# Kernel optimization log

Hardware: AMD Instinct MI355X
Metric: run time of the kernel (lower is better)

Reference implementation:

```python
import jax, jax.numpy as jnp
import numpy as np

B, S, D, H, E, F = 4, 2048, 1024, 16, 8, 4096
CAP_FACTOR = 1.25
DH = D // H


def setup_inputs() -> dict:
    key = jax.random.key(0)
    ks = jax.random.split(key, 8)
    s = 0.02
    return {
        "src": jax.random.normal(ks[0], (B, S, D), jnp.float32),
        "src_pad_mask": jnp.zeros((B, S), jnp.bool_),  # True = padding
        "ln1_g": jnp.ones((D,), jnp.float32),
        "ln1_b": jnp.zeros((D,), jnp.float32),
        "in_proj_w": jax.random.normal(ks[1], (3 * D, D), jnp.float32) * s,
        "in_proj_b": jnp.zeros((3 * D,), jnp.float32),
        "out_proj_w": jax.random.normal(ks[2], (D, D), jnp.float32) * s,
        "out_proj_b": jnp.zeros((D,), jnp.float32),
        "ln2_g": jnp.ones((D,), jnp.float32),
        "ln2_b": jnp.zeros((D,), jnp.float32),
        "router_w": jax.random.normal(ks[3], (D, E), jnp.float32) * s,
        "router_b": jnp.zeros((E,), jnp.float32),
        "w1": jax.random.normal(ks[4], (E, D, F), jnp.float32) * s,
        "b1": jnp.zeros((E, F), jnp.float32),
        "w2": jax.random.normal(ks[5], (E, F, D), jnp.float32) * s,
        "b2": jnp.zeros((E, D), jnp.float32),
    }


def _layernorm(x, g, b, eps=1e-5):
    m = jnp.mean(x, axis=-1, keepdims=True)
    v = jnp.mean(jnp.square(x - m), axis=-1, keepdims=True)
    return (x - m) * jax.lax.rsqrt(v + eps) * g + b


def _mha(x, pad_mask, in_proj_w, in_proj_b, out_proj_w, out_proj_b):
    qkv = x @ in_proj_w.T + in_proj_b                      # [B,S,3D]
    q, k, v = jnp.split(qkv, 3, axis=-1)
    q = q.reshape(B, S, H, DH)
    k = k.reshape(B, S, H, DH)
    v = v.reshape(B, S, H, DH)
    scores = jnp.einsum('bqhd,bkhd->bhqk', q, k) / np.sqrt(DH).astype(np.float32)
    scores = jnp.where(pad_mask[:, None, None, :], jnp.float32(-1e9), scores)
    attn = jax.nn.softmax(scores, axis=-1)
    out = jnp.einsum('bhqk,bkhd->bqhd', attn, v).reshape(B, S, D)
    return out @ out_proj_w.T + out_proj_b


def _switch(x, token_mask, router_w, router_b, w1, b1, w2, b2):
    N = B * S
    cap = int(CAP_FACTOR * N / E)
    tokens = x.reshape(N, D)
    tm = token_mask.reshape(N).astype(jnp.float32)
    logits = tokens @ router_w + router_b                  # [N,E]
    probs = jax.nn.softmax(logits, axis=-1)
    eidx = jnp.argmax(probs, axis=-1)                      # [N] top-1 expert
    gate = jnp.take_along_axis(probs, eidx[:, None], axis=1)[:, 0]
    oh = jax.nn.one_hot(eidx, E, dtype=jnp.float32) * tm[:, None]
    # position of each token within its expert's queue (1-based; 0 if masked)
    pos = jnp.sum(jnp.cumsum(oh, axis=0) * oh, axis=-1)
    keep = (pos > 0) & (pos <= cap)
    slot = eidx * cap + (pos - 1).astype(jnp.int32)        # flat slot in [E*cap)
    slot_scatter = jnp.where(keep, slot, E * cap)          # out-of-range => dropped
    keepf = keep.astype(jnp.float32)
    dispatch = jnp.zeros((E * cap, D), jnp.float32).at[slot_scatter].set(
        tokens * keepf[:, None], mode='drop')
    d = dispatch.reshape(E, cap, D)
    h = jax.nn.relu(jnp.einsum('ecd,edf->ecf', d, w1) + b1[:, None, :])
    o = jnp.einsum('ecf,efd->ecd', h, w2) + b2[:, None, :]
    slot_gather = jnp.where(keep, slot, 0)
    out = o.reshape(E * cap, D)[slot_gather] * (gate * keepf)[:, None]
    # aux losses over valid tokens
    denom = jnp.maximum(jnp.sum(tm), 1.0)
    f = jnp.sum(oh, axis=0) / denom                        # dispatch fraction per expert
    P = jnp.sum(probs * tm[:, None], axis=0) / denom       # mean router prob per expert
    lb_loss = E * jnp.sum(f * P)
    z_loss = jnp.sum(jnp.square(jax.nn.logsumexp(logits, axis=-1)) * tm) / denom
    return out.reshape(B, S, D), lb_loss, z_loss


def reference(src, src_pad_mask, ln1_g, ln1_b, in_proj_w, in_proj_b,
              out_proj_w, out_proj_b, ln2_g, ln2_b, router_w, router_b,
              w1, b1, w2, b2):
    x = _layernorm(src, ln1_g, ln1_b)
    attn = _mha(x, src_pad_mask, in_proj_w, in_proj_b, out_proj_w, out_proj_b)
    src1 = src + attn                                      # dropout=0.0
    token_mask = ~src_pad_mask
    x2 = _layernorm(src1, ln2_g, ln2_b)
    ffn, lb_loss, z_loss = _switch(x2, token_mask, router_w, router_b, w1, b1, w2, b2)
    src2 = src1 + ffn
    return (src2, lb_loss, z_loss)
```

## Files before the change

kernel.cpp:

```cpp
#include <hip/hip_runtime.h>

constexpr int cB = 4, cS = 2048, cD = 1024, cH = 16, cE = 8, cF = 4096;
constexpr int cN = cB * cS;
constexpr int cDH = 64;
constexpr int cCAP = 1280;
constexpr int cECAP = cE * cCAP;

typedef __attribute__((ext_vector_type(8))) short bf16x8;
typedef __attribute__((ext_vector_type(4))) float f32x4;
typedef __attribute__((ext_vector_type(4))) unsigned short u16x4;

__device__ inline unsigned short bf16_rne(float x) {
  unsigned u = __float_as_uint(x);
  u += 0x7FFF + ((u >> 16) & 1);
  return (unsigned short)(u >> 16);
}
__device__ inline float bf16_f(unsigned short h) {
  return __uint_as_float(((unsigned)h) << 16);
}

__global__ __launch_bounds__(256) void ln_kernel(const float* __restrict__ x,
                                                 const float* __restrict__ g,
                                                 const float* __restrict__ bb,
                                                 float* __restrict__ y) {
  __shared__ float red[8];
  const int row = blockIdx.x;
  const int t = threadIdx.x;
  const float4 v = ((const float4*)(x + (size_t)row * cD))[t];
  float s = v.x + v.y + v.z + v.w;
#pragma unroll
  for (int m = 32; m >= 1; m >>= 1) s += __shfl_xor(s, m, 64);
  if ((t & 63) == 0) red[t >> 6] = s;
  __syncthreads();
  const float mean = (red[0] + red[1] + red[2] + red[3]) * (1.0f / cD);
  const float dx = v.x - mean, dy = v.y - mean, dz = v.z - mean, dw = v.w - mean;
  float ss = dx * dx + dy * dy + dz * dz + dw * dw;
#pragma unroll
  for (int m = 32; m >= 1; m >>= 1) ss += __shfl_xor(ss, m, 64);
  if ((t & 63) == 0) red[4 + (t >> 6)] = ss;
  __syncthreads();
  const float var = (red[4] + red[5] + red[6] + red[7]) * (1.0f / cD);
  const float inv = rsqrtf(var + 1e-5f);
  const float4 gg = ((const float4*)g)[t];
  const float4 b4 = ((const float4*)bb)[t];
  float4 o;
  o.x = dx * inv * gg.x + b4.x;
  o.y = dy * inv * gg.y + b4.y;
  o.z = dz * inv * gg.z + b4.z;
  o.w = dw * inv * gg.w + b4.w;
  ((float4*)(y + (size_t)row * cD))[t] = o;
}

__global__ __launch_bounds__(256) void ln_split_kernel(
    const float* __restrict__ x, const float* __restrict__ g,
    const float* __restrict__ bb, unsigned short* __restrict__ yh,
    unsigned short* __restrict__ yl) {
  __shared__ float red[8];
  const int row = blockIdx.x;
  const int t = threadIdx.x;
  const float4 v = ((const float4*)(x + (size_t)row * cD))[t];
  float s = v.x + v.y + v.z + v.w;
#pragma unroll
  for (int m = 32; m >= 1; m >>= 1) s += __shfl_xor(s, m, 64);
  if ((t & 63) == 0) red[t >> 6] = s;
  __syncthreads();
  const float mean = (red[0] + red[1] + red[2] + red[3]) * (1.0f / cD);
  const float dx = v.x - mean, dy = v.y - mean, dz = v.z - mean, dw = v.w - mean;
  float ss = dx * dx + dy * dy + dz * dz + dw * dw;
#pragma unroll
  for (int m = 32; m >= 1; m >>= 1) ss += __shfl_xor(ss, m, 64);
  if ((t & 63) == 0) red[4 + (t >> 6)] = ss;
  __syncthreads();
  const float var = (red[4] + red[5] + red[6] + red[7]) * (1.0f / cD);
  const float inv = rsqrtf(var + 1e-5f);
  const float4 gg = ((const float4*)g)[t];
  const float4 b4 = ((const float4*)bb)[t];
  const float oa[4] = {dx * inv * gg.x + b4.x, dy * inv * gg.y + b4.y,
                       dz * inv * gg.z + b4.z, dw * inv * gg.w + b4.w};
  u16x4 hh, ll;
#pragma unroll
  for (int i = 0; i < 4; i++) {
    const unsigned short h16 = bf16_rne(oa[i]);
    hh[i] = h16;
    ll[i] = bf16_rne(oa[i] - bf16_f(h16));
  }
  *(u16x4*)(yh + (size_t)row * cD + t * 4) = hh;
  *(u16x4*)(yl + (size_t)row * cD + t * 4) = ll;
}

__global__ __launch_bounds__(256) void wsplit_kernel(const float* __restrict__ in,
                                                     unsigned short* __restrict__ hi,
                                                     unsigned short* __restrict__ lo,
                                                     int n4) {
  const int i = blockIdx.x * 256 + threadIdx.x;
  if (i >= n4) return;
  const float4 v = ((const float4*)in)[i];
  const float a[4] = {v.x, v.y, v.z, v.w};
  u16x4 hh, ll;
#pragma unroll
  for (int j = 0; j < 4; j++) {
    const unsigned short h16 = bf16_rne(a[j]);
    hh[j] = h16;
    ll[j] = bf16_rne(a[j] - bf16_f(h16));
  }
  *(u16x4*)(hi + (size_t)i * 4) = hh;
  *(u16x4*)(lo + (size_t)i * 4) = ll;
}

__global__ __launch_bounds__(256) void transpose_bf16_kernel(
    const float* __restrict__ in, unsigned short* __restrict__ outp, int Rr,
    int Cc) {
  __shared__ float T[64][65];
  const int z = blockIdx.z;
  in += (size_t)z * Rr * Cc;
  outp += (size_t)z * Rr * Cc;
  const int c0 = blockIdx.x * 64, r0 = blockIdx.y * 64;
  const int tid = threadIdx.x;
#pragma unroll
  for (int u = 0; u < 4; u++) {
    const int a = tid + u * 256;
    const int r = a >> 4, c4 = (a & 15) << 2;
    const float4 v = *(const float4*)(in + (size_t)(r0 + r) * Cc + c0 + c4);
    T[r][c4 + 0] = v.x;
    T[r][c4 + 1] = v.y;
    T[r][c4 + 2] = v.z;
    T[r][c4 + 3] = v.w;
  }
  __syncthreads();
#pragma unroll
  for (int u = 0; u < 4; u++) {
    const int a = tid + u * 256;
    const int c = a >> 4, r4 = (a & 15) << 2;
    u16x4 o;
#pragma unroll
    for (int i = 0; i < 4; i++) o[i] = bf16_rne(T[r4 + i][c]);
    *(u16x4*)(outp + (size_t)(c0 + c) * Rr + r0 + r4) = o;
  }
}

template <bool SPLIT, bool RELU, bool RESID, bool OUTBF16>
__global__ __launch_bounds__(256) void gemm_bf16(
    const unsigned short* __restrict__ Ah, const unsigned short* __restrict__ Al,
    size_t sA,
    const unsigned short* __restrict__ Bh, const unsigned short* __restrict__ Bl,
    size_t sB,
    const float* __restrict__ bias, size_t sBias,
    const float* __restrict__ R,
    void* __restrict__ Cv, size_t sC,
    int K, int lda, int ldb, int ldc) {
  __shared__ unsigned short AsH[128 * 40];
  __shared__ unsigned short BsH[128 * 40];
  __shared__ unsigned short AsL[SPLIT ? 128 * 40 : 8];
  __shared__ unsigned short BsL[SPLIT ? 128 * 40 : 8];
  const int z = blockIdx.z;
  Ah += (size_t)z * sA;
  Bh += (size_t)z * sB;
  if constexpr (SPLIT) {
    Al += (size_t)z * sA;
    Bl += (size_t)z * sB;
  }
  bias += (size_t)z * sBias;
  const int n0 = blockIdx.x * 128, m0 = blockIdx.y * 128;
  const int tid = threadIdx.x;
  const int wid = tid >> 6, lane = tid & 63;
  const int ln = lane & 15, quad = lane >> 4;
  const int wm = (wid >> 1) * 64, wn = (wid & 1) * 64;

  f32x4 acc[4][4];
#pragma unroll
  for (int i = 0; i < 4; i++)
#pragma unroll
    for (int j = 0; j < 4; j++) acc[i][j] = (f32x4){0.f, 0.f, 0.f, 0.f};

  for (int k0 = 0; k0 < K; k0 += 32) {
    __syncthreads();
#pragma unroll
    for (int u = 0; u < 2; u++) {
      const int c = tid + u * 256;
      const int row = c >> 2, ko = (c & 3) << 3;
      const int ld = row * 40 + ko;
      *(uint4*)&AsH[ld] = *(const uint4*)(Ah + (size_t)(m0 + row) * lda + k0 + ko);
      *(uint4*)&BsH[ld] = *(const uint4*)(Bh + (size_t)(n0 + row) * ldb + k0 + ko);
      if constexpr (SPLIT) {
        *(uint4*)&AsL[ld] = *(const uint4*)(Al + (size_t)(m0 + row) * lda + k0 + ko);
        *(uint4*)&BsL[ld] = *(const uint4*)(Bl + (size_t)(n0 + row) * ldb + k0 + ko);
      }
    }
    __syncthreads();
    bf16x8 bh[4], bl[4];
#pragma unroll
    for (int nt = 0; nt < 4; nt++) {
      bh[nt] = *(const bf16x8*)&BsH[(wn + nt * 16 + ln) * 40 + quad * 8];
      if constexpr (SPLIT)
        bl[nt] = *(const bf16x8*)&BsL[(wn + nt * 16 + ln) * 40 + quad * 8];
    }
#pragma unroll
    for (int mt = 0; mt < 4; mt++) {
      const bf16x8 ah = *(const bf16x8*)&AsH[(wm + mt * 16 + ln) * 40 + quad * 8];
      bf16x8 al;
      if constexpr (SPLIT)
        al = *(const bf16x8*)&AsL[(wm + mt * 16 + ln) * 40 + quad * 8];
#pragma unroll
      for (int nt = 0; nt < 4; nt++) {
        acc[mt][nt] =
            __builtin_amdgcn_mfma_f32_16x16x32_bf16(ah, bh[nt], acc[mt][nt], 0, 0, 0);
        if constexpr (SPLIT) {
          acc[mt][nt] =
              __builtin_amdgcn_mfma_f32_16x16x32_bf16(al, bh[nt], acc[mt][nt], 0, 0, 0);
          acc[mt][nt] =
              __builtin_amdgcn_mfma_f32_16x16x32_bf16(ah, bl[nt], acc[mt][nt], 0, 0, 0);
        }
      }
    }
  }
  float* Cf = nullptr;
  unsigned short* Cb = nullptr;
  if constexpr (OUTBF16)
    Cb = (unsigned short*)Cv + (size_t)z * sC;
  else
    Cf = (float*)Cv + (size_t)z * sC;
#pragma unroll
  for (int mt = 0; mt < 4; mt++) {
#pragma unroll
    for (int nt = 0; nt < 4; nt++) {
      const int col = n0 + wn + nt * 16 + ln;
      const float bv = bias[col];
#pragma unroll
      for (int r = 0; r < 4; r++) {
        const int row = m0 + wm + mt * 16 + quad * 4 + r;
        float v = acc[mt][nt][r] + bv;
        if constexpr (RELU) v = fmaxf(v, 0.f);
        if constexpr (RESID) v += R[(size_t)row * ldc + col];
        if constexpr (OUTBF16)
          Cb[(size_t)row * ldc + col] = bf16_rne(v);
        else
          Cf[(size_t)row * ldc + col] = v;
      }
    }
  }
}

__global__ __launch_bounds__(256) void qkv_split_kernel(
    const float* __restrict__ qkv,
    unsigned short* __restrict__ Qh, unsigned short* __restrict__ Ql,
    unsigned short* __restrict__ Kh, unsigned short* __restrict__ Kl,
    unsigned short* __restrict__ Vth, unsigned short* __restrict__ Vtl) {
  __shared__ float Vs[64 * 66];
  const int s0 = blockIdx.x << 6;
  const int h = blockIdx.y, b = blockIdx.z;
  const int tid = threadIdx.x;
  const size_t qkbase = ((size_t)(b * cH + h) * cS + s0) * cDH;
  const size_t vtbase = (size_t)(b * cH + h) * cDH * cS + s0;
#pragma unroll
  for (int u = 0; u < 4; u++) {
    const int a = tid + u * 256;
    const int r = a >> 4, c4 = (a & 15) << 2;
    const float* rowp = qkv + (size_t)(b * cS + s0 + r) * (3 * cD) + h * cDH + c4;
    const float4 qv = *(const float4*)(rowp);
    const float4 kv = *(const float4*)(rowp + cD);
    const float4 vv = *(const float4*)(rowp + 2 * cD);
    u16x4 hq, lq, hk, lk;
    const float qa[4] = {qv.x, qv.y, qv.z, qv.w};
    const float ka[4] = {kv.x, kv.y, kv.z, kv.w};
    const float va[4] = {vv.x, vv.y, vv.z, vv.w};
#pragma unroll
    for (int i = 0; i < 4; i++) {
      const unsigned short h16 = bf16_rne(qa[i]);
      hq[i] = h16;
      lq[i] = bf16_rne(qa[i] - bf16_f(h16));
      const unsigned short h17 = bf16_rne(ka[i]);
      hk[i] = h17;
      lk[i] = bf16_rne(ka[i] - bf16_f(h17));
      Vs[(c4 + i) * 66 + r] = va[i];
    }
    *(u16x4*)(Qh + qkbase + (size_t)r * cDH + c4) = hq;
    *(u16x4*)(Ql + qkbase + (size_t)r * cDH + c4) = lq;
    *(u16x4*)(Kh + qkbase + (size_t)r * cDH + c4) = hk;
    *(u16x4*)(Kl + qkbase + (size_t)r * cDH + c4) = lk;
  }
  __syncthreads();
#pragma unroll
  for (int u = 0; u < 4; u++) {
    const int a = tid + u * 256;
    const int dh = a >> 4, k4 = (a & 15) << 2;
    u16x4 hv, lv;
#pragma unroll
    for (int i = 0; i < 4; i++) {
      const float x = Vs[dh * 66 + k4 + i];
      const unsigned short h16 = bf16_rne(x);
      hv[i] = h16;
      lv[i] = bf16_rne(x - bf16_f(h16));
    }
    *(u16x4*)(Vth + vtbase + (size_t)dh * cS + k4) = hv;
    *(u16x4*)(Vtl + vtbase + (size_t)dh * cS + k4) = lv;
  }
}

__global__ __launch_bounds__(256) void attn_mfma_kernel(
    const unsigned short* __restrict__ Qh, const unsigned short* __restrict__ Ql,
    const unsigned short* __restrict__ Kh, const unsigned short* __restrict__ Kl,
    const unsigned short* __restrict__ Vth, const unsigned short* __restrict__ Vtl,
    const unsigned char* __restrict__ pad, unsigned short* __restrict__ Oh,
    unsigned short* __restrict__ Ol) {
  __shared__ unsigned short KsH[64 * 72];
  __shared__ unsigned short KsL[64 * 72];
  __shared__ unsigned short VsH[64 * 72];
  __shared__ unsigned short VsL[64 * 72];
  __shared__ unsigned short PsH[4 * 16 * 72];
  __shared__ unsigned short PsL[4 * 16 * 72];
  __shared__ float Mk[64];

  const int q0 = blockIdx.x << 6;
  const int h = blockIdx.y, b = blockIdx.z;
  const int tid = threadIdx.x;
  const int wid = tid >> 6, lane = tid & 63;
  const int ln = lane & 15, quad = lane >> 4;
  constexpr float SC2 = 0.125f * 1.4426950408889634f;

  const size_t bh = (size_t)(b * cH + h);
  const unsigned short* gKh = Kh + bh * cS * cDH;
  const unsigned short* gKl = Kl + bh * cS * cDH;
  const unsigned short* gVh = Vth + bh * cDH * cS;
  const unsigned short* gVl = Vtl + bh * cDH * cS;

  const size_t qbase = (bh * cS + q0 + wid * 16 + ln) * cDH;
  bf16x8 qh[2], ql[2];
#pragma unroll
  for (int ks = 0; ks < 2; ks++) {
    qh[ks] = *(const bf16x8*)(Qh + qbase + ks * 32 + quad * 8);
    ql[ks] = *(const bf16x8*)(Ql + qbase + ks * 32 + quad * 8);
  }

  f32x4 Oc[4];
  float mprev[4], lrun[4];
#pragma unroll
  for (int dt = 0; dt < 4; dt++) Oc[dt] = (f32x4){0.f, 0.f, 0.f, 0.f};
#pragma unroll
  for (int r = 0; r < 4; r++) {
    mprev[r] = -1e30f;
    lrun[r] = 0.f;
  }

  for (int kt = 0; kt < cS / 64; kt++) {
    const int k0 = kt << 6;
    __syncthreads();
#pragma unroll
    for (int u = 0; u < 2; u++) {
      const int a = tid + (u << 8);
      const int row = a >> 3, c8 = (a & 7) << 3;
      const int ld = row * 72 + c8;
      *(uint4*)&KsH[ld] = *(const uint4*)(gKh + (size_t)(k0 + row) * cDH + c8);
      *(uint4*)&KsL[ld] = *(const uint4*)(gKl + (size_t)(k0 + row) * cDH + c8);
      *(uint4*)&VsH[ld] = *(const uint4*)(gVh + (size_t)row * cS + k0 + c8);
      *(uint4*)&VsL[ld] = *(const uint4*)(gVl + (size_t)row * cS + k0 + c8);
    }
    if (tid < 64) Mk[tid] = pad[b * cS + k0 + tid] ? -1e30f : 0.0f;
    __syncthreads();

    f32x4 sac[4];
#pragma unroll
    for (int st = 0; st < 4; st++) {
      f32x4 acc = (f32x4){0.f, 0.f, 0.f, 0.f};
      const unsigned short* krH = &KsH[(st * 16 + ln) * 72];
      const unsigned short* krL = &KsL[(st * 16 + ln) * 72];
#pragma unroll
      for (int ks = 0; ks < 2; ks++) {
        const bf16x8 kh = *(const bf16x8*)(krH + ks * 32 + quad * 8);
        const bf16x8 kl = *(const bf16x8*)(krL + ks * 32 + quad * 8);
        acc = __builtin_amdgcn_mfma_f32_16x16x32_bf16(qh[ks], kh, acc, 0, 0, 0);
        acc = __builtin_amdgcn_mfma_f32_16x16x32_bf16(ql[ks], kh, acc, 0, 0, 0);
        acc = __builtin_amdgcn_mfma_f32_16x16x32_bf16(qh[ks], kl, acc, 0, 0, 0);
      }
      sac[st] = acc;
    }
    float sf[4][4];
#pragma unroll
    for (int st = 0; st < 4; st++) {
      const float ma = Mk[st * 16 + ln];
#pragma unroll
      for (int r = 0; r < 4; r++) sf[st][r] = sac[st][r] * SC2 + ma;
    }
#pragma unroll
    for (int r = 0; r < 4; r++) {
      float vm = fmaxf(fmaxf(sf[0][r], sf[1][r]), fmaxf(sf[2][r], sf[3][r]));
      vm = fmaxf(vm, __shfl_xor(vm, 1, 64));
      vm = fmaxf(vm, __shfl_xor(vm, 2, 64));
      vm = fmaxf(vm, __shfl_xor(vm, 4, 64));
      vm = fmaxf(vm, __shfl_xor(vm, 8, 64));
      const float mnew = fmaxf(mprev[r], vm);
      const float alpha = exp2f(mprev[r] - mnew);
      float rs = 0.f;
      unsigned short ph[4], pl[4];
#pragma unroll
      for (int st = 0; st < 4; st++) {
        const float p = exp2f(sf[st][r] - mnew);
        rs += p;
        const unsigned short h16 = bf16_rne(p);
        ph[st] = h16;
        pl[st] = bf16_rne(p - bf16_f(h16));
      }
      rs += __shfl_xor(rs, 1, 64);
      rs += __shfl_xor(rs, 2, 64);
      rs += __shfl_xor(rs, 4, 64);
      rs += __shfl_xor(rs, 8, 64);
      lrun[r] = lrun[r] * alpha + rs;
      mprev[r] = mnew;
#pragma unroll
      for (int dt = 0; dt < 4; dt++) Oc[dt][r] *= alpha;
      const int prow = wid * 1152 + (quad * 4 + r) * 72 + ln;
#pragma unroll
      for (int st = 0; st < 4; st++) {
        PsH[prow + st * 16] = ph[st];
        PsL[prow + st * 16] = pl[st];
      }
    }
    const unsigned short* pwH = PsH + wid * 1152 + ln * 72;
    const unsigned short* pwL = PsL + wid * 1152 + ln * 72;
#pragma unroll
    for (int dt = 0; dt < 4; dt++) {
      f32x4 acc = Oc[dt];
      const unsigned short* vrH = &VsH[(dt * 16 + ln) * 72];
      const unsigned short* vrL = &VsL[(dt * 16 + ln) * 72];
#pragma unroll
      for (int ks = 0; ks < 2; ks++) {
        const bf16x8 phv = *(const bf16x8*)(pwH + ks * 32 + quad * 8);
        const bf16x8 plv = *(const bf16x8*)(pwL + ks * 32 + quad * 8);
        const bf16x8 vh = *(const bf16x8*)(vrH + ks * 32 + quad * 8);
        const bf16x8 vl = *(const bf16x8*)(vrL + ks * 32 + quad * 8);
        acc = __builtin_amdgcn_mfma_f32_16x16x32_bf16(phv, vh, acc, 0, 0, 0);
        acc = __builtin_amdgcn_mfma_f32_16x16x32_bf16(plv, vh, acc, 0, 0, 0);
        acc = __builtin_amdgcn_mfma_f32_16x16x32_bf16(phv, vl, acc, 0, 0, 0);
      }
      Oc[dt] = acc;
    }
  }
  float inv[4];
#pragma unroll
  for (int r = 0; r < 4; r++) inv[r] = 1.0f / lrun[r];
#pragma unroll
  for (int dt = 0; dt < 4; dt++) {
#pragma unroll
    for (int r = 0; r < 4; r++) {
      const int tok = b * cS + q0 + wid * 16 + quad * 4 + r;
      const float v = Oc[dt][r] * inv[r];
      const unsigned short h16 = bf16_rne(v);
      const size_t idx = (size_t)tok * cD + h * cDH + dt * 16 + ln;
      Oh[idx] = h16;
      Ol[idx] = bf16_rne(v - bf16_f(h16));
    }
  }
}

__global__ __launch_bounds__(256) void router_kernel(
    const float* __restrict__ x2, const float* __restrict__ rw,
    const float* __restrict__ rb, const unsigned char* __restrict__ pad,
    float* __restrict__ gate, int* __restrict__ eidx, float* __restrict__ Psum,
    float* __restrict__ zsum) {
  __shared__ float Pacc[8];
  __shared__ float Zacc;
  if (threadIdx.x < 8) Pacc[threadIdx.x] = 0.f;
  if (threadIdx.x == 8) Zacc = 0.f;
  __syncthreads();
  const int tid = threadIdx.x, wid = tid >> 6, lane = tid & 63;
  const int e = lane & 7, dbase = lane >> 3;
  for (int tok = blockIdx.x * 4 + wid; tok < cN; tok += gridDim.x * 4) {
    const float* xr = x2 + (size_t)tok * cD;
    float partial = 0.f;
#pragma unroll 8
    for (int i = 0; i < cD / 8; i++) {
      const int d = dbase + i * 8;
      partial += xr[d] * rw[d * 8 + e];
    }
    partial += __shfl_xor(partial, 8, 64);
    partial += __shfl_xor(partial, 16, 64);
    partial += __shfl_xor(partial, 32, 64);
    const float logit = partial + rb[e];
    float mx = logit;
    mx = fmaxf(mx, __shfl_xor(mx, 1, 64));
    mx = fmaxf(mx, __shfl_xor(mx, 2, 64));
    mx = fmaxf(mx, __shfl_xor(mx, 4, 64));
    const float ex = __expf(logit - mx);
    float sm = ex;
    sm += __shfl_xor(sm, 1, 64);
    sm += __shfl_xor(sm, 2, 64);
    sm += __shfl_xor(sm, 4, 64);
    const float prob = ex / sm;
    float bv = logit;
    int bi = e;
#pragma unroll
    for (int m = 1; m < 8; m <<= 1) {
      const float ov = __shfl_xor(bv, m, 64);
      const int oi = __shfl_xor(bi, m, 64);
      if (ov > bv || (ov == bv && oi < bi)) {
        bv = ov;
        bi = oi;
      }
    }
    const float g = __shfl(prob, (lane & 0x38) | bi, 64);
    const bool valid = (pad[tok] == 0);
    if (lane == 0) {
      eidx[tok] = bi;
      gate[tok] = g;
    }
    if (valid) {
      if (lane < 8) atomicAdd(&Pacc[lane], prob);
      if (lane == 0) {
        const float lse = mx + logf(sm);
        atomicAdd(&Zacc, lse * lse);
      }
    }
  }
  __syncthreads();
  if (threadIdx.x < 8) atomicAdd(&Psum[threadIdx.x], Pacc[threadIdx.x]);
  if (threadIdx.x == 8) atomicAdd(zsum, Zacc);
}

__global__ __launch_bounds__(256) void scan_kernel(const int* __restrict__ eidx,
                                                   const unsigned char* __restrict__ pad,
                                                   int* __restrict__ slot,
                                                   int* __restrict__ counts) {
  __shared__ int cnt[256][8];
  const int t = threadIdx.x;
  int lc[8] = {0, 0, 0, 0, 0, 0, 0, 0};
  const int base = t * 32;
  for (int i = 0; i < 32; i++) {
    const int tok = base + i;
    if (!pad[tok]) lc[eidx[tok]]++;
  }
#pragma unroll
  for (int e2 = 0; e2 < 8; e2++) cnt[t][e2] = lc[e2];
  __syncthreads();
  if (t < 8) {
    int run = 0;
    for (int i = 0; i < 256; i++) {
      const int v = cnt[i][t];
      cnt[i][t] = run;
      run += v;
    }
    counts[t] = run;
  }
  __syncthreads();
  int off[8];
#pragma unroll
  for (int e2 = 0; e2 < 8; e2++) off[e2] = cnt[t][e2];
  for (int i = 0; i < 32; i++) {
    const int tok = base + i;
    if (!pad[tok]) {
      const int e2 = eidx[tok];
      const int p = off[e2]++;
      slot[tok] = (p < cCAP) ? (e2 * cCAP + p) : -1;
    } else {
      slot[tok] = -1;
    }
  }
}

__global__ __launch_bounds__(256) void dispatch_bf16_kernel(
    const float* __restrict__ x2, const int* __restrict__ slot,
    unsigned short* __restrict__ disp) {
  const int tok = blockIdx.x;
  const int s = slot[tok];
  if (s < 0) return;
  const float4 v = ((const float4*)(x2 + (size_t)tok * cD))[threadIdx.x];
  u16x4 o;
  o[0] = bf16_rne(v.x);
  o[1] = bf16_rne(v.y);
  o[2] = bf16_rne(v.z);
  o[3] = bf16_rne(v.w);
  *(u16x4*)(disp + (size_t)s * cD + threadIdx.x * 4) = o;
}

__global__ __launch_bounds__(256) void gather_kernel(const float* __restrict__ src1,
                                                     const float* __restrict__ o,
                                                     const int* __restrict__ slot,
                                                     const float* __restrict__ gate,
                                                     float* __restrict__ out) {
  const int tok = blockIdx.x;
  float4 r = ((const float4*)(src1 + (size_t)tok * cD))[threadIdx.x];
  const int s = slot[tok];
  if (s >= 0) {
    const float g = gate[tok];
    const float4 ov = ((const float4*)(o + (size_t)s * cD))[threadIdx.x];
    r.x += g * ov.x;
    r.y += g * ov.y;
    r.z += g * ov.z;
    r.w += g * ov.w;
  }
  ((float4*)(out + (size_t)tok * cD))[threadIdx.x] = r;
}

__global__ void loss_kernel(const int* __restrict__ counts,
                            const float* __restrict__ Psum,
                            const float* __restrict__ zsum,
                            float* __restrict__ out) {
  if (threadIdx.x == 0) {
    int tot = 0;
    for (int e2 = 0; e2 < 8; e2++) tot += counts[e2];
    const float denom = fmaxf((float)tot, 1.0f);
    float lp = 0.f;
    for (int e2 = 0; e2 < 8; e2++)
      lp += ((float)counts[e2] / denom) * (Psum[e2] / denom);
    out[0] = 8.0f * lp;
    out[1] = zsum[0] / denom;
  }
}

constexpr size_t OFF_A = 0;
constexpr size_t OFF_B = 25165824;
constexpr size_t OFF_XHL = 50331648;
constexpr size_t OFF_SRC1 = 58720256;
constexpr size_t OFF_X2O = 67108864;
constexpr size_t OFF_IPW = 77594624;
constexpr size_t OFF_OPW = 80740352;
constexpr size_t OFF_MISC = 81788928;

extern "C" void kernel_launch(void* const* d_in, const int* in_sizes, int n_in,
                              void* d_out, int out_size, void* d_ws, size_t ws_size,
                              hipStream_t stream) {
  (void)in_sizes; (void)n_in; (void)out_size; (void)ws_size;
  const float* src = (const float*)d_in[0];
  const unsigned char* pad = (const unsigned char*)d_in[1];
  const float* ln1_g = (const float*)d_in[2];
  const float* ln1_b = (const float*)d_in[3];
  const float* in_proj_w = (const float*)d_in[4];
  const float* in_proj_b = (const float*)d_in[5];
  const float* out_proj_w = (const float*)d_in[6];
  const float* out_proj_b = (const float*)d_in[7];
  const float* ln2_g = (const float*)d_in[8];
  const float* ln2_b = (const float*)d_in[9];
  const float* router_w = (const float*)d_in[10];
  const float* router_b = (const float*)d_in[11];
  const float* w1 = (const float*)d_in[12];
  const float* b1 = (const float*)d_in[13];
  const float* w2 = (const float*)d_in[14];
  const float* b2 = (const float*)d_in[15];
  float* out = (float*)d_out;
  float* w = (float*)d_ws;

  float* qkv = w + OFF_A;
  unsigned short* w1t = (unsigned short*)(w + OFF_A);
  unsigned short* w2t = (unsigned short*)(w + OFF_A);
  unsigned short* usB = (unsigned short*)(w + OFF_B);
  constexpr size_t SPN = (size_t)cN * cD;
  unsigned short* Qh = usB + 0 * SPN;
  unsigned short* Ql = usB + 1 * SPN;
  unsigned short* Kh = usB + 2 * SPN;
  unsigned short* Kl = usB + 3 * SPN;
  unsigned short* Vth = usB + 4 * SPN;
  unsigned short* Vtl = usB + 5 * SPN;
  unsigned short* hbuf16 = usB;
  unsigned short* xh = (unsigned short*)(w + OFF_XHL);
  unsigned short* xl = xh + SPN;
  unsigned short* Oh = xh;
  unsigned short* Ol = xh + SPN;
  unsigned short* disp16 = xh;
  float* src1 = w + OFF_SRC1;
  float* x2 = w + OFF_X2O;
  float* obuf = w + OFF_X2O;
  unsigned short* ipwh = (unsigned short*)(w + OFF_IPW);
  unsigned short* ipwl = ipwh + (size_t)3 * cD * cD;
  unsigned short* opwh = (unsigned short*)(w + OFF_OPW);
  unsigned short* opwl = opwh + (size_t)cD * cD;
  float* gate = w + OFF_MISC;
  int* eidx = (int*)(w + OFF_MISC + 8192);
  int* slot = (int*)(w + OFF_MISC + 16384);
  float* Psum = w + OFF_MISC + 24576;
  float* zsum = Psum + 8;
  int* counts = (int*)(Psum + 16);

  hipMemsetAsync(Psum, 0, 9 * sizeof(float), stream);

  ln_split_kernel<<<cN, 256, 0, stream>>>(src, ln1_g, ln1_b, xh, xl);
  wsplit_kernel<<<3072, 256, 0, stream>>>(in_proj_w, ipwh, ipwl, 786432);
  wsplit_kernel<<<1024, 256, 0, stream>>>(out_proj_w, opwh, opwl, 262144);
  gemm_bf16<true, false, false, false><<<dim3(24, 64, 1), 256, 0, stream>>>(
      xh, xl, 0, ipwh, ipwl, 0, in_proj_b, 0, nullptr, qkv, 0,
      cD, cD, cD, 3 * cD);
  qkv_split_kernel<<<dim3(cS / 64, cH, cB), 256, 0, stream>>>(
      qkv, Qh, Ql, Kh, Kl, Vth, Vtl);
  transpose_bf16_kernel<<<dim3(64, 16, 8), 256, 0, stream>>>(w1, w1t, cD, cF);
  attn_mfma_kernel<<<dim3(cS / 64, cH, cB), 256, 0, stream>>>(
      Qh, Ql, Kh, Kl, Vth, Vtl, pad, Oh, Ol);
  gemm_bf16<true, false, true, false><<<dim3(8, 64, 1), 256, 0, stream>>>(
      Oh, Ol, 0, opwh, opwl, 0, out_proj_b, 0, src, src1, 0,
      cD, cD, cD, cD);
  ln_kernel<<<cN, 256, 0, stream>>>(src1, ln2_g, ln2_b, x2);
  router_kernel<<<256, 256, 0, stream>>>(x2, router_w, router_b, pad, gate, eidx,
                                         Psum, zsum);
  scan_kernel<<<1, 256, 0, stream>>>(eidx, pad, slot, counts);
  dispatch_bf16_kernel<<<cN, 256, 0, stream>>>(x2, slot, disp16);
  gemm_bf16<false, true, false, true><<<dim3(32, 10, 8), 256, 0, stream>>>(
      disp16, nullptr, (size_t)cCAP * cD, w1t, nullptr, (size_t)cD * cF,
      b1, cF, nullptr, hbuf16, (size_t)cCAP * cF, cD, cD, cD, cF);
  transpose_bf16_kernel<<<dim3(16, 64, 8), 256, 0, stream>>>(w2, w2t, cF, cD);
  gemm_bf16<false, false, false, false><<<dim3(8, 10, 8), 256, 0, stream>>>(
      hbuf16, nullptr, (size_t)cCAP * cF, w2t, nullptr, (size_t)cF * cD,
      b2, cD, nullptr, obuf, (size_t)cCAP * cD, cF, cF, cF, cD);
  gather_kernel<<<cN, 256, 0, stream>>>(src1, obuf, slot, gate, out);
  loss_kernel<<<1, 64, 0, stream>>>(counts, Psum, zsum, out + (size_t)cN * cD);
}
```

Measured before the change: 1.488 ms.

## Fuse QKV split into GEMM epilogue and transpose attention MFMA operands

Measured after the change: 1.419 ms. 4.6% less time.

```diff
diff --git a/kernel.cpp b/kernel.cpp
--- a/kernel.cpp
+++ b/kernel.cpp
@@ -4,7 +4,6 @@
 constexpr int cN = cB * cS;
 constexpr int cDH = 64;
 constexpr int cCAP = 1280;
-constexpr int cECAP = cE * cCAP;
 
 typedef __attribute__((ext_vector_type(8))) short bf16x8;
 typedef __attribute__((ext_vector_type(4))) float f32x4;
@@ -138,7 +137,7 @@
   }
 }
 
-template <bool SPLIT, bool RELU, bool RESID, bool OUTBF16>
+template <bool SPLIT, bool RELU, bool RESID, int OUT>
 __global__ __launch_bounds__(256) void gemm_bf16(
     const unsigned short* __restrict__ Ah, const unsigned short* __restrict__ Al,
     size_t sA,
@@ -147,7 +146,10 @@
     const float* __restrict__ bias, size_t sBias,
     const float* __restrict__ R,
     void* __restrict__ Cv, size_t sC,
-    int K, int lda, int ldb, int ldc) {
+    int K, int lda, int ldb, int ldc,
+    unsigned short* __restrict__ Qh, unsigned short* __restrict__ Ql,
+    unsigned short* __restrict__ Kh, unsigned short* __restrict__ Kl,
+    unsigned short* __restrict__ Vth, unsigned short* __restrict__ Vtl) {
   __shared__ unsigned short AsH[128 * 40];
   __shared__ unsigned short BsH[128 * 40];
   __shared__ unsigned short AsL[SPLIT ? 128 * 40 : 8];
@@ -213,86 +215,73 @@
       }
     }
   }
-  float* Cf = nullptr;
-  unsigned short* Cb = nullptr;
-  if constexpr (OUTBF16)
-    Cb = (unsigned short*)Cv + (size_t)z * sC;
-  else
-    Cf = (float*)Cv + (size_t)z * sC;
-#pragma unroll
-  for (int mt = 0; mt < 4; mt++) {
-#pragma unroll
-    for (int nt = 0; nt < 4; nt++) {
-      const int col = n0 + wn + nt * 16 + ln;
-      const float bv = bias[col];
-#pragma unroll
-      for (int r = 0; r < 4; r++) {
-        const int row = m0 + wm + mt * 16 + quad * 4 + r;
-        float v = acc[mt][nt][r] + bv;
-        if constexpr (RELU) v = fmaxf(v, 0.f);
-        if constexpr (RESID) v += R[(size_t)row * ldc + col];
-        if constexpr (OUTBF16)
-          Cb[(size_t)row * ldc + col] = bf16_rne(v);
-        else
-          Cf[(size_t)row * ldc + col] = v;
-      }
-    }
-  }
-}
-
-__global__ __launch_bounds__(256) void qkv_split_kernel(
-    const float* __restrict__ qkv,
-    unsigned short* __restrict__ Qh, unsigned short* __restrict__ Ql,
-    unsigned short* __restrict__ Kh, unsigned short* __restrict__ Kl,
-    unsigned short* __restrict__ Vth, unsigned short* __restrict__ Vtl) {
-  __shared__ float Vs[64 * 66];
-  const int s0 = blockIdx.x << 6;
-  const int h = blockIdx.y, b = blockIdx.z;
-  const int tid = threadIdx.x;
-  const size_t qkbase = ((size_t)(b * cH + h) * cS + s0) * cDH;
-  const size_t vtbase = (size_t)(b * cH + h) * cDH * cS + s0;
-#pragma unroll
-  for (int u = 0; u < 4; u++) {
-    const int a = tid + u * 256;
-    const int r = a >> 4, c4 = (a & 15) << 2;
-    const float* rowp = qkv + (size_t)(b * cS + s0 + r) * (3 * cD) + h * cDH + c4;
-    const float4 qv = *(const float4*)(rowp);
-    const float4 kv = *(const float4*)(rowp + cD);
-    const float4 vv = *(const float4*)(rowp + 2 * cD);
-    u16x4 hq, lq, hk, lk;
-    const float qa[4] = {qv.x, qv.y, qv.z, qv.w};
-    const float ka[4] = {kv.x, kv.y, kv.z, kv.w};
-    const float va[4] = {vv.x, vv.y, vv.z, vv.w};
-#pragma unroll
-    for (int i = 0; i < 4; i++) {
-      const unsigned short h16 = bf16_rne(qa[i]);
-      hq[i] = h16;
-      lq[i] = bf16_rne(qa[i] - bf16_f(h16));
-      const unsigned short h17 = bf16_rne(ka[i]);
-      hk[i] = h17;
-      lk[i] = bf16_rne(ka[i] - bf16_f(h17));
-      Vs[(c4 + i) * 66 + r] = va[i];
-    }
-    *(u16x4*)(Qh + qkbase + (size_t)r * cDH + c4) = hq;
-    *(u16x4*)(Ql + qkbase + (size_t)r * cDH + c4) = lq;
-    *(u16x4*)(Kh + qkbase + (size_t)r * cDH + c4) = hk;
-    *(u16x4*)(Kl + qkbase + (size_t)r * cDH + c4) = lk;
-  }
-  __syncthreads();
-#pragma unroll
-  for (int u = 0; u < 4; u++) {
-    const int a = tid + u * 256;
-    const int dh = a >> 4, k4 = (a & 15) << 2;
-    u16x4 hv, lv;
-#pragma unroll
-    for (int i = 0; i < 4; i++) {
-      const float x = Vs[dh * 66 + k4 + i];
-      const unsigned short h16 = bf16_rne(x);
-      hv[i] = h16;
-      lv[i] = bf16_rne(x - bf16_f(h16));
-    }
-    *(u16x4*)(Vth + vtbase + (size_t)dh * cS + k4) = hv;
-    *(u16x4*)(Vtl + vtbase + (size_t)dh * cS + k4) = lv;
+  if constexpr (OUT == 2) {
+#pragma unroll
+    for (int mt = 0; mt < 4; mt++) {
+      const int row0 = m0 + wm + mt * 16 + quad * 4;
+      const int b_ = row0 >> 11, s0_ = row0 & 2047;
+      const size_t bbase = (size_t)b_ * cH * cS * cDH;
+#pragma unroll
+      for (int nt = 0; nt < 4; nt++) {
+        const int col = n0 + wn + nt * 16 + ln;
+        const float bv = bias[col];
+        const int sec = col >> 10;
+        const int f = col & 1023;
+        const int hh = f >> 6, d = f & 63;
+        const size_t bh_off = bbase + (size_t)hh * cS * cDH;
+        float vals[4];
+#pragma unroll
+        for (int r = 0; r < 4; r++) vals[r] = acc[mt][nt][r] + bv;
+        if (sec == 2) {
+          u16x4 hi4, lo4;
+#pragma unroll
+          for (int r = 0; r < 4; r++) {
+            const unsigned short h16 = bf16_rne(vals[r]);
+            hi4[r] = h16;
+            lo4[r] = bf16_rne(vals[r] - bf16_f(h16));
+          }
+          const size_t idx = bh_off + (size_t)d * cS + s0_;
+          *(u16x4*)(Vth + idx) = hi4;
+          *(u16x4*)(Vtl + idx) = lo4;
+        } else {
+          unsigned short* dsth = (sec == 0) ? Qh : Kh;
+          unsigned short* dstl = (sec == 0) ? Ql : Kl;
+#pragma unroll
+          for (int r = 0; r < 4; r++) {
+            const unsigned short h16 = bf16_rne(vals[r]);
+            const size_t idx = bh_off + (size_t)(s0_ + r) * cDH + d;
+            dsth[idx] = h16;
+            dstl[idx] = bf16_rne(vals[r] - bf16_f(h16));
+          }
+        }
+      }
+    }
+  } else {
+    float* Cf = nullptr;
+    unsigned short* Cb = nullptr;
+    if constexpr (OUT == 1)
+      Cb = (unsigned short*)Cv + (size_t)z * sC;
+    else
+      Cf = (float*)Cv + (size_t)z * sC;
+#pragma unroll
+    for (int mt = 0; mt < 4; mt++) {
+#pragma unroll
+      for (int nt = 0; nt < 4; nt++) {
+        const int col = n0 + wn + nt * 16 + ln;
+        const float bv = bias[col];
+#pragma unroll
+        for (int r = 0; r < 4; r++) {
+          const int row = m0 + wm + mt * 16 + quad * 4 + r;
+          float v = acc[mt][nt][r] + bv;
+          if constexpr (RELU) v = fmaxf(v, 0.f);
+          if constexpr (RESID) v += R[(size_t)row * ldc + col];
+          if constexpr (OUT == 1)
+            Cb[(size_t)row * ldc + col] = bf16_rne(v);
+          else
+            Cf[(size_t)row * ldc + col] = v;
+        }
+      }
+    }
   }
 }
 
@@ -332,14 +321,9 @@
   }
 
   f32x4 Oc[4];
-  float mprev[4], lrun[4];
 #pragma unroll
   for (int dt = 0; dt < 4; dt++) Oc[dt] = (f32x4){0.f, 0.f, 0.f, 0.f};
-#pragma unroll
-  for (int r = 0; r < 4; r++) {
-    mprev[r] = -1e30f;
-    lrun[r] = 0.f;
-  }
+  float mprev = -1e30f, lrun = 0.f;
 
   for (int kt = 0; kt < cS / 64; kt++) {
     const int k0 = kt << 6;
@@ -357,7 +341,7 @@
     if (tid < 64) Mk[tid] = pad[b * cS + k0 + tid] ? -1e30f : 0.0f;
     __syncthreads();
 
-    f32x4 sac[4];
+    float sf[4][4];
 #pragma unroll
     for (int st = 0; st < 4; st++) {
       f32x4 acc = (f32x4){0.f, 0.f, 0.f, 0.f};
@@ -367,52 +351,54 @@
       for (int ks = 0; ks < 2; ks++) {
         const bf16x8 kh = *(const bf16x8*)(krH + ks * 32 + quad * 8);
         const bf16x8 kl = *(const bf16x8*)(krL + ks * 32 + quad * 8);
-        acc = __builtin_amdgcn_mfma_f32_16x16x32_bf16(qh[ks], kh, acc, 0, 0, 0);
-        acc = __builtin_amdgcn_mfma_f32_16x16x32_bf16(ql[ks], kh, acc, 0, 0, 0);
-        acc = __builtin_amdgcn_mfma_f32_16x16x32_bf16(qh[ks], kl, acc, 0, 0, 0);
-      }
-      sac[st] = acc;
-    }
-    float sf[4][4];
+        acc = __builtin_amdgcn_mfma_f32_16x16x32_bf16(kh, qh[ks], acc, 0, 0, 0);
+        acc = __builtin_amdgcn_mfma_f32_16x16x32_bf16(kl, qh[ks], acc, 0, 0, 0);
+        acc = __builtin_amdgcn_mfma_f32_16x16x32_bf16(kh, ql[ks], acc, 0, 0, 0);
+      }
+      const float4 mkv = *(const float4*)&Mk[st * 16 + quad * 4];
+      sf[st][0] = acc[0] * SC2 + mkv.x;
+      sf[st][1] = acc[1] * SC2 + mkv.y;
+      sf[st][2] = acc[2] * SC2 + mkv.z;
+      sf[st][3] = acc[3] * SC2 + mkv.w;
+    }
+    float vm = -1e30f;
+#pragma unroll
+    for (int st = 0; st < 4; st++)
+#pragma unroll
+      for (int r = 0; r < 4; r++) vm = fmaxf(vm, sf[st][r]);
+    vm = fmaxf(vm, __shfl_xor(vm, 16, 64));
+    vm = fmaxf(vm, __shfl_xor(vm, 32, 64));
+    const float mnew = fmaxf(mprev, vm);
+    const float alpha = exp2f(mprev - mnew);
+    float rs = 0.f;
+    u16x4 phv[4], plv[4];
 #pragma unroll
     for (int st = 0; st < 4; st++) {
-      const float ma = Mk[st * 16 + ln];
-#pragma unroll
-      for (int r = 0; r < 4; r++) sf[st][r] = sac[st][r] * SC2 + ma;
-    }
-#pragma unroll
-    for (int r = 0; r < 4; r++) {
-      float vm = fmaxf(fmaxf(sf[0][r], sf[1][r]), fmaxf(sf[2][r], sf[3][r]));
-      vm = fmaxf(vm, __shfl_xor(vm, 1, 64));
-      vm = fmaxf(vm, __shfl_xor(vm, 2, 64));
-      vm = fmaxf(vm, __shfl_xor(vm, 4, 64));
-      vm = fmaxf(vm, __shfl_xor(vm, 8, 64));
-      const float mnew = fmaxf(mprev[r], vm);
-      const float alpha = exp2f(mprev[r] - mnew);
-      float rs = 0.f;
-      unsigned short ph[4], pl[4];
-#pragma unroll
-      for (int st = 0; st < 4; st++) {
+#pragma unroll
+      for (int r = 0; r < 4; r++) {
         const float p = exp2f(sf[st][r] - mnew);
         rs += p;
         const unsigned short h16 = bf16_rne(p);
-        ph[st] = h16;
-        pl[st] = bf16_rne(p - bf16_f(h16));
-      }
-      rs += __shfl_xor(rs, 1, 64);
-      rs += __shfl_xor(rs, 2, 64);
-      rs += __shfl_xor(rs, 4, 64);
-      rs += __shfl_xor(rs, 8, 64);
-      lrun[r] = lrun[r] * alpha + rs;
-      mprev[r] = mnew;
-#pragma unroll
-      for (int dt = 0; dt < 4; dt++) Oc[dt][r] *= alpha;
-      const int prow = wid * 1152 + (quad * 4 + r) * 72 + ln;
-#pragma unroll
-      for (int st = 0; st < 4; st++) {
-        PsH[prow + st * 16] = ph[st];
-        PsL[prow + st * 16] = pl[st];
-      }
+        phv[st][r] = h16;
+        plv[st][r] = bf16_rne(p - bf16_f(h16));
+      }
+    }
+    rs += __shfl_xor(rs, 16, 64);
+    rs += __shfl_xor(rs, 32, 64);
+    lrun = lrun * alpha + rs;
+    mprev = mnew;
+#pragma unroll
+    for (int dt = 0; dt < 4; dt++) {
+      Oc[dt][0] *= alpha;
+      Oc[dt][1] *= alpha;
+      Oc[dt][2] *= alpha;
+      Oc[dt][3] *= alpha;
+    }
+    const int pbase = wid * 1152 + ln * 72 + quad * 4;
+#pragma unroll
+    for (int st = 0; st < 4; st++) {
+      *(u16x4*)&PsH[pbase + st * 16] = phv[st];
+      *(u16x4*)&PsL[pbase + st * 16] = plv[st];
     }
     const unsigned short* pwH = PsH + wid * 1152 + ln * 72;
     const unsigned short* pwL = PsL + wid * 1152 + ln * 72;
@@ -423,31 +409,32 @@
       const unsigned short* vrL = &VsL[(dt * 16 + ln) * 72];
 #pragma unroll
       for (int ks = 0; ks < 2; ks++) {
-        const bf16x8 phv = *(const bf16x8*)(pwH + ks * 32 + quad * 8);
-        const bf16x8 plv = *(const bf16x8*)(pwL + ks * 32 + quad * 8);
         const bf16x8 vh = *(const bf16x8*)(vrH + ks * 32 + quad * 8);
         const bf16x8 vl = *(const bf16x8*)(vrL + ks * 32 + quad * 8);
-        acc = __builtin_amdgcn_mfma_f32_16x16x32_bf16(phv, vh, acc, 0, 0, 0);
-        acc = __builtin_amdgcn_mfma_f32_16x16x32_bf16(plv, vh, acc, 0, 0, 0);
-        acc = __builtin_amdgcn_mfma_f32_16x16x32_bf16(phv, vl, acc, 0, 0, 0);
+        const bf16x8 pbh = *(const bf16x8*)(pwH + ks * 32 + quad * 8);
+        const bf16x8 pbl = *(const bf16x8*)(pwL + ks * 32 + quad * 8);
+        acc = __builtin_amdgcn_mfma_f32_16x16x32_bf16(vh, pbh, acc, 0, 0, 0);
+        acc = __builtin_amdgcn_mfma_f32_16x16x32_bf16(vh, pbl, acc, 0, 0, 0);
+        acc = __builtin_amdgcn_mfma_f32_16x16x32_bf16(vl, pbh, acc, 0, 0, 0);
       }
       Oc[dt] = acc;
     }
   }
-  float inv[4];
-#pragma unroll
-  for (int r = 0; r < 4; r++) inv[r] = 1.0f / lrun[r];
+  const float inv = 1.0f / lrun;
+  const int tok = b * cS + q0 + wid * 16 + ln;
 #pragma unroll
   for (int dt = 0; dt < 4; dt++) {
+    u16x4 oh4, ol4;
 #pragma unroll
     for (int r = 0; r < 4; r++) {
-      const int tok = b * cS + q0 + wid * 16 + quad * 4 + r;
-      const float v = Oc[dt][r] * inv[r];
+      const float v = Oc[dt][r] * inv;
       const unsigned short h16 = bf16_rne(v);
-      const size_t idx = (size_t)tok * cD + h * cDH + dt * 16 + ln;
-      Oh[idx] = h16;
-      Ol[idx] = bf16_rne(v - bf16_f(h16));
-    }
+      oh4[r] = h16;
+      ol4[r] = bf16_rne(v - bf16_f(h16));
+    }
+    const size_t idx = (size_t)tok * cD + h * cDH + dt * 16 + quad * 4;
+    *(u16x4*)(Oh + idx) = oh4;
+    *(u16x4*)(Ol + idx) = ol4;
   }
 }
 
@@ -637,7 +624,6 @@
   float* out = (float*)d_out;
   float* w = (float*)d_ws;
 
-  float* qkv = w + OFF_A;
   unsigned short* w1t = (unsigned short*)(w + OFF_A);
   unsigned short* w2t = (unsigned short*)(w + OFF_A);
   unsigned short* usB = (unsigned short*)(w + OFF_B);
@@ -673,29 +659,29 @@
   ln_split_kernel<<<cN, 256, 0, stream>>>(src, ln1_g, ln1_b, xh, xl);
   wsplit_kernel<<<3072, 256, 0, stream>>>(in_proj_w, ipwh, ipwl, 786432);
   wsplit_kernel<<<1024, 256, 0, stream>>>(out_proj_w, opwh, opwl, 262144);
-  gemm_bf16<true, false, false, false><<<dim3(24, 64, 1), 256, 0, stream>>>(
-      xh, xl, 0, ipwh, ipwl, 0, in_proj_b, 0, nullptr, qkv, 0,
-      cD, cD, cD, 3 * cD);
-  qkv_split_kernel<<<dim3(cS / 64, cH, cB), 256, 0, stream>>>(
-      qkv, Qh, Ql, Kh, Kl, Vth, Vtl);
+  gemm_bf16<true, false, false, 2><<<dim3(24, 64, 1), 256, 0, stream>>>(
+      xh, xl, 0, ipwh, ipwl, 0, in_proj_b, 0, nullptr, nullptr, 0,
+      cD, cD, cD, 0, Qh, Ql, Kh, Kl, Vth, Vtl);
   transpose_bf16_kernel<<<dim3(64, 16, 8), 256, 0, stream>>>(w1, w1t, cD, cF);
   attn_mfma_kernel<<<dim3(cS / 64, cH, cB), 256, 0, stream>>>(
       Qh, Ql, Kh, Kl, Vth, Vtl, pad, Oh, Ol);
-  gemm_bf16<true, false, true, false><<<dim3(8, 64, 1), 256, 0, stream>>>(
+  gemm_bf16<true, false, true, 0><<<dim3(8, 64, 1), 256, 0, stream>>>(
       Oh, Ol, 0, opwh, opwl, 0, out_proj_b, 0, src, src1, 0,
-      cD, cD, cD, cD);
+      cD, cD, cD, cD, nullptr, nullptr, nullptr, nullptr, nullptr, nullptr);
   ln_kernel<<<cN, 256, 0, stream>>>(src1, ln2_g, ln2_b, x2);
   router_kernel<<<256, 256, 0, stream>>>(x2, router_w, router_b, pad, gate, eidx,
                                          Psum, zsum);
   scan_kernel<<<1, 256, 0, stream>>>(eidx, pad, slot, counts);
   dispatch_bf16_kernel<<<cN, 256, 0, stream>>>(x2, slot, disp16);
-  gemm_bf16<false, true, false, true><<<dim3(32, 10, 8), 256, 0, stream>>>(
+  gemm_bf16<false, true, false, 1><<<dim3(32, 10, 8), 256, 0, stream>>>(
       disp16, nullptr, (size_t)cCAP * cD, w1t, nullptr, (size_t)cD * cF,
-      b1, cF, nullptr, hbuf16, (size_t)cCAP * cF, cD, cD, cD, cF);
+      b1, cF, nullptr, hbuf16, (size_t)cCAP * cF, cD, cD, cD, cF,
+      nullptr, nullptr, nullptr, nullptr, nullptr, nullptr);
   transpose_bf16_kernel<<<dim3(16, 64, 8), 256, 0, stream>>>(w2, w2t, cF, cD);
-  gemm_bf16<false, false, false, false><<<dim3(8, 10, 8), 256, 0, stream>>>(
+  gemm_bf16<false, false, false, 0><<<dim3(8, 10, 8), 256, 0, stream>>>(
       hbuf16, nullptr, (size_t)cCAP * cF, w2t, nullptr, (size_t)cF * cD,
-      b2, cD, nullptr, obuf, (size_t)cCAP * cD, cF, cF, cF, cD);
+      b2, cD, nullptr, obuf, (size_t)cCAP * cD, cF, cF, cF, cD,
+      nullptr, nullptr, nullptr, nullptr, nullptr, nullptr);
   gather_kernel<<<cN, 256, 0, stream>>>(src1, obuf, slot, gate, out);
   loss_kernel<<<1, 64, 0, stream>>>(counts, Psum, zsum, out + (size_t)cN * cD);
 }
```
